# Performance work log

Measured on AMD Instinct MI355X. Metric: run time of the kernel, lower is better.

Reference implementation:

```python
import jax, jax.numpy as jnp
import numpy as np


def setup_inputs() -> dict:
    key = jax.random.key(0)
    k1, k2, k3, k4, k5 = jax.random.split(key, 5)
    B, S, I, N = 64, 512, 2, 2048
    scale = (1.0 / N) ** 0.5
    velocities = jax.random.normal(k1, (B, S, I), dtype=jnp.float32)
    h0 = jax.random.uniform(k2, (B, N), dtype=jnp.float32)
    W_lin = jax.random.normal(k3, (N, I), dtype=jnp.float32) * scale
    b_lin = jax.random.normal(k4, (N,), dtype=jnp.float32) * scale
    W_rec = jax.random.normal(k5, (N, N), dtype=jnp.float32) * scale
    return {"velocities": velocities, "h0": h0, "W_lin": W_lin,
            "b_lin": b_lin, "W_rec": W_rec}


def reference(velocities, h0, W_lin, b_lin, W_rec):
    # velocities: [B, S, 2]; h0: [B, N]; W_lin: [N, 2]; b_lin: [N]; W_rec: [N, N]
    # base_logits = Linear(velocities): [B, S, N]
    base_logits = jnp.einsum('bsi,ni->bsn', velocities, W_lin) + b_lin

    def step(h, logits_t):
        # logits_t: [B, N]; h: [B, N] (probabilities)
        z = logits_t + h @ W_rec
        h_new = jax.nn.softmax(z, axis=-1)
        return h_new, h_new

    # scan over time axis S
    _, outs = jax.lax.scan(step, h0, jnp.swapaxes(base_logits, 0, 1))
    # outs: [S, B, N] -> [B, S, N]
    return jnp.swapaxes(outs, 0, 1)
```

## Files before the change

kernel.cpp:

```cpp
#include <hip/hip_runtime.h>
#include <stdint.h>

typedef __attribute__((ext_vector_type(8))) short short8;
typedef __attribute__((ext_vector_type(4))) float floatx4;
typedef __attribute__((ext_vector_type(4))) unsigned int uintx4;

static constexpr int kB = 64, kS = 512, kN = 2048;

static constexpr size_t PART_OFF   = 0;
static constexpr size_t PART_BYTES = (size_t)4 * 16 * 64 * 4;
static constexpr size_t EBUF_OFF   = 16384;
static constexpr size_t SLAB_ELEMS = (size_t)kB * kN;

__device__ __forceinline__ unsigned short f2bf(float x) {
    unsigned u = __builtin_bit_cast(unsigned, x);
    u = (u + 0x7fffu + ((u >> 16) & 1u)) >> 16;
    return (unsigned short)u;
}

__global__ __launch_bounds__(256) void pcn(
    const float* __restrict__ vel, const float* __restrict__ h0,
    const float* __restrict__ Wlin, const float* __restrict__ blin,
    const float* __restrict__ Wrec, float* __restrict__ out,
    float* part, unsigned short* ebuf)
{
    extern __shared__ char smem[];
    short8* Wlds = (short8*)smem;
    float*  red  = (float*)(smem + 131072);
    float*  red2 = (float*)(smem + 147456);

    const int tid  = threadIdx.x;
    const int lane = tid & 63;
    const int w    = tid >> 6;
    const int bg   = (blockIdx.x & 7) >> 1;
    const int cg   = ((blockIdx.x >> 3) << 1) | (blockIdx.x & 1);
    const int b0   = bg * 16;
    const int c0   = cg * 32;
    const int koff = (lane >> 4) << 3;

    const int r   = tid >> 4;
    const int c16 = tid & 15;
    const int cc  = c16 * 2;

    {
        const float a0 = h0[(size_t)(b0 + r) * kN + c0 + cc];
        const float a1 = h0[(size_t)(b0 + r) * kN + c0 + cc + 1];
        const unsigned pk = (unsigned)f2bf(a0) | ((unsigned)f2bf(a1) << 16);
        __hip_atomic_store((unsigned*)(ebuf + (size_t)(b0 + r) * kN + c0 + cc), pk,
                           __ATOMIC_RELAXED, __HIP_MEMORY_SCOPE_AGENT);
    }

    for (int kt = w * 16; kt < w * 16 + 16; ++kt) {
        for (int ct = 0; ct < 2; ++ct) {
            const int colg = c0 + ct * 16 + (lane & 15);
            const int kb   = kt * 32 + koff;
            short8 v;
            #pragma unroll
            for (int j = 0; j < 8; ++j)
                v[j] = (short)f2bf(Wrec[(size_t)(kb + j) * kN + colg]);
            Wlds[(kt * 2 + ct) * 64 + lane] = v;
        }
    }

    const float wl00 = Wlin[(c0 + cc) * 2 + 0],     wl01 = Wlin[(c0 + cc) * 2 + 1];
    const float wl10 = Wlin[(c0 + cc + 1) * 2 + 0], wl11 = Wlin[(c0 + cc + 1) * 2 + 1];
    const float bl0  = blin[c0 + cc], bl1 = blin[c0 + cc + 1];

    __syncthreads();

    short8 onesB;
    #pragma unroll
    for (int j = 0; j < 8; ++j) onesB[j] = (short)0x3F80;

    const int arow = b0 + (lane & 15);
    const char* const abase0 =
        (const char*)ebuf + 2 * ((size_t)arow * kN + w * 512 + koff);

    float prev_e0 = 0.f, prev_e1 = 0.f;

#define PCN_LD(i, ofs) \
    asm volatile("global_load_dwordx4 %0, %1, off offset:" #ofs \
                 : "=v"(tmp[i]) : "v"(aptr))
#define PCN_RLD(i, ofs) \
    if (((tmp[i][0] | tmp[i][1] | tmp[i][2] | tmp[i][3]) >> 31) != 0) \
        asm volatile("global_load_dwordx4 %0, %1, off offset:" #ofs " sc0 sc1" \
                     : "=v"(tmp[i]) : "v"(aptr))

    for (int t = 0; t < kS; ++t) {
        const float2 vv = *(const float2*)(vel + ((size_t)(b0 + r) * kS + t) * 2);
        const char* aptr = abase0 + (size_t)t * (SLAB_ELEMS * 2);

        uintx4 tmp[16];
        PCN_LD(0, 0);    PCN_LD(1, 64);   PCN_LD(2, 128);  PCN_LD(3, 192);
        PCN_LD(4, 256);  PCN_LD(5, 320);  PCN_LD(6, 384);  PCN_LD(7, 448);
        PCN_LD(8, 512);  PCN_LD(9, 576);  PCN_LD(10, 640); PCN_LD(11, 704);
        PCN_LD(12, 768); PCN_LD(13, 832); PCN_LD(14, 896); PCN_LD(15, 960);
        asm volatile("s_waitcnt vmcnt(0)" ::: "memory");
        __builtin_amdgcn_sched_barrier(0);
        {
            int spin = 0;
            for (;;) {
                unsigned bad = 0;
                #pragma unroll
                for (int kt = 0; kt < 16; ++kt)
                    bad |= tmp[kt][0] | tmp[kt][1] | tmp[kt][2] | tmp[kt][3];
                if (__all((int)((bad >> 31) == 0))) break;
                if (++spin > (1 << 16)) break;
                if (spin > 2) __builtin_amdgcn_s_sleep(1);
                PCN_RLD(0, 0);    PCN_RLD(1, 64);   PCN_RLD(2, 128);  PCN_RLD(3, 192);
                PCN_RLD(4, 256);  PCN_RLD(5, 320);  PCN_RLD(6, 384);  PCN_RLD(7, 448);
                PCN_RLD(8, 512);  PCN_RLD(9, 576);  PCN_RLD(10, 640); PCN_RLD(11, 704);
                PCN_RLD(12, 768); PCN_RLD(13, 832); PCN_RLD(14, 896); PCN_RLD(15, 960);
                asm volatile("s_waitcnt vmcnt(0)" ::: "memory");
                __builtin_amdgcn_sched_barrier(0);
            }
        }
        __builtin_amdgcn_sched_barrier(0);

        floatx4 acc0 = {0.f,0.f,0.f,0.f}, acc1 = {0.f,0.f,0.f,0.f},
                acc2 = {0.f,0.f,0.f,0.f};
        #pragma unroll
        for (int kt = 0; kt < 16; ++kt) {
            const int ktg = w * 16 + kt;
            const short8 bq0 = Wlds[(ktg * 2 + 0) * 64 + lane];
            const short8 bq1 = Wlds[(ktg * 2 + 1) * 64 + lane];
            const short8 a   = __builtin_bit_cast(short8, tmp[kt]);
            acc0 = __builtin_amdgcn_mfma_f32_16x16x32_bf16(a, bq0, acc0, 0, 0, 0);
            acc1 = __builtin_amdgcn_mfma_f32_16x16x32_bf16(a, bq1, acc1, 0, 0, 0);
            acc2 = __builtin_amdgcn_mfma_f32_16x16x32_bf16(a, onesB, acc2, 0, 0, 0);
        }

        float* redb  = red  + (t & 1) * 2048;
        float* red2b = red2 + (t & 1) * 1024;
        {
            const int ccol = lane & 15, crow = (lane >> 4) * 4;
            #pragma unroll
            for (int i = 0; i < 4; ++i) {
                redb[w * 512 + (crow + i) * 32 + ccol]      = acc0[i];
                redb[w * 512 + (crow + i) * 32 + 16 + ccol] = acc1[i];
                red2b[w * 256 + (crow + i) * 16 + ccol]     = acc2[i];
            }
        }
        __builtin_amdgcn_sched_barrier(0);
        asm volatile("s_waitcnt lgkmcnt(0)" ::: "memory");
        __builtin_amdgcn_s_barrier();
        __builtin_amdgcn_sched_barrier(0);

        float g0 = 0.f, g1 = 0.f, sr = 0.f;
        {
            const int cell = tid * 2;
            #pragma unroll
            for (int ww = 0; ww < 4; ++ww) {
                g0 += redb[ww * 512 + cell];
                g1 += redb[ww * 512 + cell + 1];
                sr += red2b[ww * 256 + tid];
            }
        }
        const float s_inv = (t == 0) ? 1.0f : 1.0f / sr;

        const float z0 = fmaf(g0, s_inv, fmaf(vv.x, wl00, fmaf(vv.y, wl01, bl0)));
        const float z1 = fmaf(g1, s_inv, fmaf(vv.x, wl10, fmaf(vv.y, wl11, bl1)));
        const float e0 = __expf(z0), e1 = __expf(z1);

        if (t < kS - 1) {
            const unsigned pk = (unsigned)f2bf(e0) | ((unsigned)f2bf(e1) << 16);
            __hip_atomic_store(
                (unsigned*)(ebuf + (size_t)(t + 1) * SLAB_ELEMS + (size_t)(b0 + r) * kN + c0 + cc),
                pk, __ATOMIC_RELAXED, __HIP_MEMORY_SCOPE_AGENT);
        }
        if (t > 0) {
            float2 o; o.x = prev_e0 * s_inv; o.y = prev_e1 * s_inv;
            *(float2*)(out + ((size_t)(b0 + r) * kS + (t - 1)) * kN + c0 + cc) = o;
        }
        prev_e0 = e0; prev_e1 = e1;
    }

    float es = prev_e0 + prev_e1;
    es += __shfl_xor(es, 8, 16);
    es += __shfl_xor(es, 4, 16);
    es += __shfl_xor(es, 2, 16);
    es += __shfl_xor(es, 1, 16);
    if (c16 == 0)
        __hip_atomic_store(part + ((size_t)bg * 16 + r) * 64 + cg, es,
                           __ATOMIC_RELAXED, __HIP_MEMORY_SCOPE_AGENT);
    float p0, p1, p2, p3;
    {
        const float* fpb = part + ((size_t)bg * 16 + r) * 64 + c16 * 4;
        bool rdy = false;
        int spin = 0;
        do {
            p0 = __hip_atomic_load(fpb + 0, __ATOMIC_RELAXED, __HIP_MEMORY_SCOPE_AGENT);
            p1 = __hip_atomic_load(fpb + 1, __ATOMIC_RELAXED, __HIP_MEMORY_SCOPE_AGENT);
            p2 = __hip_atomic_load(fpb + 2, __ATOMIC_RELAXED, __HIP_MEMORY_SCOPE_AGENT);
            p3 = __hip_atomic_load(fpb + 3, __ATOMIC_RELAXED, __HIP_MEMORY_SCOPE_AGENT);
            rdy = (p0 != 0.f) & (p1 != 0.f) & (p2 != 0.f) & (p3 != 0.f);
            if (++spin > (1 << 16)) break;
            if (spin > 8) __builtin_amdgcn_s_sleep(1);
        } while (!__all((int)rdy));
    }
    float s = (p0 + p1) + (p2 + p3);
    s += __shfl_xor(s, 8, 16);
    s += __shfl_xor(s, 4, 16);
    s += __shfl_xor(s, 2, 16);
    s += __shfl_xor(s, 1, 16);
    const float sf = 1.0f / s;
    {
        float2 o; o.x = prev_e0 * sf; o.y = prev_e1 * sf;
        *(float2*)(out + ((size_t)(b0 + r) * kS + (kS - 1)) * kN + c0 + cc) = o;
    }
}

extern "C" void kernel_launch(void* const* d_in, const int* in_sizes, int n_in,
                              void* d_out, int out_size, void* d_ws, size_t ws_size,
                              hipStream_t stream)
{
    (void)in_sizes; (void)n_in; (void)out_size; (void)ws_size;
    const float* vel  = (const float*)d_in[0];
    const float* h0   = (const float*)d_in[1];
    const float* Wlin = (const float*)d_in[2];
    const float* blin = (const float*)d_in[3];
    const float* Wrec = (const float*)d_in[4];
    float* out = (float*)d_out;

    char* ws = (char*)d_ws;
    float* part          = (float*)(ws + PART_OFF);
    unsigned short* ebuf = (unsigned short*)(ws + EBUF_OFF);

    (void)hipMemsetAsync(ws + PART_OFF, 0, PART_BYTES, stream);

    const unsigned smem = 131072 + 16384 + 8192;
    (void)hipFuncSetAttribute((const void*)pcn,
        hipFuncAttributeMaxDynamicSharedMemorySize, (int)smem);

    void* args[] = { (void*)&vel, (void*)&h0, (void*)&Wlin, (void*)&blin,
                     (void*)&Wrec, (void*)&out, (void*)&part, (void*)&ebuf };
    hipError_t err = hipLaunchCooperativeKernel((const void*)pcn,
        dim3(256), dim3(256), args, smem, stream);
    if (err != hipSuccess) {
        (void)hipGetLastError();
        hipLaunchKernelGGL(pcn, dim3(256), dim3(256), smem, stream,
                           vel, h0, Wlin, blin, Wrec, out, part, ebuf);
    }
}
```

Baseline: 2.611 ms.

## Publish per-block softmax partial sums via global flags instead of ones-MFMA row sums

Each block now reduces its exp values per row with shuffles and writes the partial sum to a per-timestep slot in a global flag array. Consumers poll those slots, whose sign bit doubles as a readiness gate, and add them up, instead of running a third MFMA against a ones vector on the bf16 activations. This removes a third of the MFMAs per step and the matching LDS traffic, and it makes the denominator an fp32 sum of unrounded values. In exchange it adds a polling loop and extra global atomics every step, and it drops the memset, so it assumes the workspace starts with the sign bit set.

```diff
diff --git a/kernel.cpp b/kernel.cpp
--- a/kernel.cpp
+++ b/kernel.cpp
@@ -7,9 +7,9 @@
 
 static constexpr int kB = 64, kS = 512, kN = 2048;
 
-static constexpr size_t PART_OFF   = 0;
-static constexpr size_t PART_BYTES = (size_t)4 * 16 * 64 * 4;
-static constexpr size_t EBUF_OFF   = 16384;
+static constexpr size_t FLAG_OFF   = 0;
+static constexpr size_t FLAG_ROUND = (size_t)4 * 16 * 64;
+static constexpr size_t EBUF_OFF   = (size_t)(kS + 1) * FLAG_ROUND * 4;
 static constexpr size_t SLAB_ELEMS = (size_t)kB * kN;
 
 __device__ __forceinline__ unsigned short f2bf(float x) {
@@ -22,7 +22,7 @@
     const float* __restrict__ vel, const float* __restrict__ h0,
     const float* __restrict__ Wlin, const float* __restrict__ blin,
     const float* __restrict__ Wrec, float* __restrict__ out,
-    float* part, unsigned short* ebuf)
+    float* flags, unsigned short* ebuf)
 {
     extern __shared__ char smem[];
     short8* Wlds = (short8*)smem;
@@ -48,6 +48,9 @@
         const unsigned pk = (unsigned)f2bf(a0) | ((unsigned)f2bf(a1) << 16);
         __hip_atomic_store((unsigned*)(ebuf + (size_t)(b0 + r) * kN + c0 + cc), pk,
                            __ATOMIC_RELAXED, __HIP_MEMORY_SCOPE_AGENT);
+        if (c16 == 0)
+            __hip_atomic_store(flags + ((size_t)0 * 4 + bg) * 16 * 64 + (size_t)r * 64 + cg,
+                               1.0f, __ATOMIC_RELAXED, __HIP_MEMORY_SCOPE_AGENT);
     }
 
     for (int kt = w * 16; kt < w * 16 + 16; ++kt) {
@@ -68,13 +71,13 @@
 
     __syncthreads();
 
-    short8 onesB;
-    #pragma unroll
-    for (int j = 0; j < 8; ++j) onesB[j] = (short)0x3F80;
-
     const int arow = b0 + (lane & 15);
     const char* const abase0 =
         (const char*)ebuf + 2 * ((size_t)arow * kN + w * 512 + koff);
+
+    const int gr = lane >> 2;
+    const int gj = lane & 3;
+    const size_t gate_base = ((size_t)bg * 16 + gr) * 64 + (w * 16 + gj * 4);
 
     float prev_e0 = 0.f, prev_e1 = 0.f;
 
@@ -89,6 +92,26 @@
     for (int t = 0; t < kS; ++t) {
         const float2 vv = *(const float2*)(vel + ((size_t)(b0 + r) * kS + t) * 2);
         const char* aptr = abase0 + (size_t)t * (SLAB_ELEMS * 2);
+
+        float q;
+        {
+            const unsigned* fpb =
+                (const unsigned*)(flags + (size_t)t * FLAG_ROUND + gate_base);
+            unsigned u0, u1, u2, u3;
+            int spin = 0;
+            for (;;) {
+                u0 = __hip_atomic_load(fpb + 0, __ATOMIC_RELAXED, __HIP_MEMORY_SCOPE_AGENT);
+                u1 = __hip_atomic_load(fpb + 1, __ATOMIC_RELAXED, __HIP_MEMORY_SCOPE_AGENT);
+                u2 = __hip_atomic_load(fpb + 2, __ATOMIC_RELAXED, __HIP_MEMORY_SCOPE_AGENT);
+                u3 = __hip_atomic_load(fpb + 3, __ATOMIC_RELAXED, __HIP_MEMORY_SCOPE_AGENT);
+                const int ok = (int)(((u0 | u1 | u2 | u3) >> 31) == 0);
+                if (__all(ok)) break;
+                if (++spin > (1 << 16)) break;
+                if (spin > 4) __builtin_amdgcn_s_sleep(1);
+            }
+            q = __builtin_bit_cast(float, u0) + __builtin_bit_cast(float, u1) +
+                __builtin_bit_cast(float, u2) + __builtin_bit_cast(float, u3);
+        }
 
         uintx4 tmp[16];
         PCN_LD(0, 0);    PCN_LD(1, 64);   PCN_LD(2, 128);  PCN_LD(3, 192);
@@ -117,8 +140,7 @@
         }
         __builtin_amdgcn_sched_barrier(0);
 
-        floatx4 acc0 = {0.f,0.f,0.f,0.f}, acc1 = {0.f,0.f,0.f,0.f},
-                acc2 = {0.f,0.f,0.f,0.f};
+        floatx4 acc0 = {0.f,0.f,0.f,0.f}, acc1 = {0.f,0.f,0.f,0.f};
         #pragma unroll
         for (int kt = 0; kt < 16; ++kt) {
             const int ktg = w * 16 + kt;
@@ -127,19 +149,18 @@
             const short8 a   = __builtin_bit_cast(short8, tmp[kt]);
             acc0 = __builtin_amdgcn_mfma_f32_16x16x32_bf16(a, bq0, acc0, 0, 0, 0);
             acc1 = __builtin_amdgcn_mfma_f32_16x16x32_bf16(a, bq1, acc1, 0, 0, 0);
-            acc2 = __builtin_amdgcn_mfma_f32_16x16x32_bf16(a, onesB, acc2, 0, 0, 0);
         }
 
         float* redb  = red  + (t & 1) * 2048;
-        float* red2b = red2 + (t & 1) * 1024;
+        float* red2b = red2 + (t & 1) * 256;
         {
             const int ccol = lane & 15, crow = (lane >> 4) * 4;
             #pragma unroll
             for (int i = 0; i < 4; ++i) {
                 redb[w * 512 + (crow + i) * 32 + ccol]      = acc0[i];
                 redb[w * 512 + (crow + i) * 32 + 16 + ccol] = acc1[i];
-                red2b[w * 256 + (crow + i) * 16 + ccol]     = acc2[i];
-            }
+            }
+            red2b[w * 64 + lane] = q;
         }
         __builtin_amdgcn_sched_barrier(0);
         asm volatile("s_waitcnt lgkmcnt(0)" ::: "memory");
@@ -153,7 +174,8 @@
             for (int ww = 0; ww < 4; ++ww) {
                 g0 += redb[ww * 512 + cell];
                 g1 += redb[ww * 512 + cell + 1];
-                sr += red2b[ww * 256 + tid];
+                const floatx4 qv = *(const floatx4*)&red2b[ww * 64 + r * 4];
+                sr += (qv[0] + qv[1]) + (qv[2] + qv[3]);
             }
         }
         const float s_inv = (t == 0) ? 1.0f : 1.0f / sr;
@@ -161,6 +183,12 @@
         const float z0 = fmaf(g0, s_inv, fmaf(vv.x, wl00, fmaf(vv.y, wl01, bl0)));
         const float z1 = fmaf(g1, s_inv, fmaf(vv.x, wl10, fmaf(vv.y, wl11, bl1)));
         const float e0 = __expf(z0), e1 = __expf(z1);
+
+        float es = e0 + e1;
+        es += __shfl_xor(es, 8, 16);
+        es += __shfl_xor(es, 4, 16);
+        es += __shfl_xor(es, 2, 16);
+        es += __shfl_xor(es, 1, 16);
 
         if (t < kS - 1) {
             const unsigned pk = (unsigned)f2bf(e0) | ((unsigned)f2bf(e1) << 16);
@@ -168,6 +196,11 @@
                 (unsigned*)(ebuf + (size_t)(t + 1) * SLAB_ELEMS + (size_t)(b0 + r) * kN + c0 + cc),
                 pk, __ATOMIC_RELAXED, __HIP_MEMORY_SCOPE_AGENT);
         }
+        if (c16 == 0)
+            __hip_atomic_store(flags + (size_t)(t + 1) * FLAG_ROUND +
+                                   ((size_t)bg * 16 + r) * 64 + cg,
+                               es, __ATOMIC_RELAXED, __HIP_MEMORY_SCOPE_AGENT);
+
         if (t > 0) {
             float2 o; o.x = prev_e0 * s_inv; o.y = prev_e1 * s_inv;
             *(float2*)(out + ((size_t)(b0 + r) * kS + (t - 1)) * kN + c0 + cc) = o;
@@ -175,28 +208,24 @@
         prev_e0 = e0; prev_e1 = e1;
     }
 
-    float es = prev_e0 + prev_e1;
-    es += __shfl_xor(es, 8, 16);
-    es += __shfl_xor(es, 4, 16);
-    es += __shfl_xor(es, 2, 16);
-    es += __shfl_xor(es, 1, 16);
-    if (c16 == 0)
-        __hip_atomic_store(part + ((size_t)bg * 16 + r) * 64 + cg, es,
-                           __ATOMIC_RELAXED, __HIP_MEMORY_SCOPE_AGENT);
     float p0, p1, p2, p3;
     {
-        const float* fpb = part + ((size_t)bg * 16 + r) * 64 + c16 * 4;
-        bool rdy = false;
+        const unsigned* fpb = (const unsigned*)(flags + (size_t)kS * FLAG_ROUND +
+                                                ((size_t)bg * 16 + r) * 64 + c16 * 4);
+        unsigned u0, u1, u2, u3;
         int spin = 0;
-        do {
-            p0 = __hip_atomic_load(fpb + 0, __ATOMIC_RELAXED, __HIP_MEMORY_SCOPE_AGENT);
-            p1 = __hip_atomic_load(fpb + 1, __ATOMIC_RELAXED, __HIP_MEMORY_SCOPE_AGENT);
-            p2 = __hip_atomic_load(fpb + 2, __ATOMIC_RELAXED, __HIP_MEMORY_SCOPE_AGENT);
-            p3 = __hip_atomic_load(fpb + 3, __ATOMIC_RELAXED, __HIP_MEMORY_SCOPE_AGENT);
-            rdy = (p0 != 0.f) & (p1 != 0.f) & (p2 != 0.f) & (p3 != 0.f);
+        for (;;) {
+            u0 = __hip_atomic_load(fpb + 0, __ATOMIC_RELAXED, __HIP_MEMORY_SCOPE_AGENT);
+            u1 = __hip_atomic_load(fpb + 1, __ATOMIC_RELAXED, __HIP_MEMORY_SCOPE_AGENT);
+            u2 = __hip_atomic_load(fpb + 2, __ATOMIC_RELAXED, __HIP_MEMORY_SCOPE_AGENT);
+            u3 = __hip_atomic_load(fpb + 3, __ATOMIC_RELAXED, __HIP_MEMORY_SCOPE_AGENT);
+            const int ok = (int)(((u0 | u1 | u2 | u3) >> 31) == 0);
+            if (__all(ok)) break;
             if (++spin > (1 << 16)) break;
             if (spin > 8) __builtin_amdgcn_s_sleep(1);
-        } while (!__all((int)rdy));
+        }
+        p0 = __builtin_bit_cast(float, u0); p1 = __builtin_bit_cast(float, u1);
+        p2 = __builtin_bit_cast(float, u2); p3 = __builtin_bit_cast(float, u3);
     }
     float s = (p0 + p1) + (p2 + p3);
     s += __shfl_xor(s, 8, 16);
@@ -223,22 +252,21 @@
     float* out = (float*)d_out;
 
     char* ws = (char*)d_ws;
-    float* part          = (float*)(ws + PART_OFF);
+    float* flags         = (float*)(ws + FLAG_OFF);
     unsigned short* ebuf = (unsigned short*)(ws + EBUF_OFF);
 
-    (void)hipMemsetAsync(ws + PART_OFF, 0, PART_BYTES, stream);
-
-    const unsigned smem = 131072 + 16384 + 8192;
+
+    const unsigned smem = 131072 + 16384 + 2048;
     (void)hipFuncSetAttribute((const void*)pcn,
         hipFuncAttributeMaxDynamicSharedMemorySize, (int)smem);
 
     void* args[] = { (void*)&vel, (void*)&h0, (void*)&Wlin, (void*)&blin,
-                     (void*)&Wrec, (void*)&out, (void*)&part, (void*)&ebuf };
+                     (void*)&Wrec, (void*)&out, (void*)&flags, (void*)&ebuf };
     hipError_t err = hipLaunchCooperativeKernel((const void*)pcn,
         dim3(256), dim3(256), args, smem, stream);
     if (err != hipSuccess) {
         (void)hipGetLastError();
         hipLaunchKernelGGL(pcn, dim3(256), dim3(256), smem, stream,
-                           vel, h0, Wlin, blin, Wrec, out, part, ebuf);
+                           vel, h0, Wlin, blin, Wrec, out, flags, ebuf);
     }
 }
```

Result: slower. 3.678 ms (+40.9%).
